# Optimization experiments

Measured on AMD Instinct MI355X. Metric: run time of the kernel, lower is better.

The kernel has to match this reference:

```python
import jax, jax.numpy as jnp
import numpy as np

B, S, E, H = 64, 512, 1024, 1024

def setup_inputs() -> dict:
    key = jax.random.key(0)
    k1, k2, k3, k4, k5 = jax.random.split(key, 5)
    emben_x = jax.random.normal(k1, (B, S, E), dtype=jnp.float32)
    sW = 1.0 / np.sqrt(E)
    sU = 1.0 / np.sqrt(H)
    W_w = jax.random.uniform(k2, (H, E), jnp.float32, -sW, sW)
    W_b = jax.random.uniform(k3, (H,), jnp.float32, -sW, sW)
    U_w = jax.random.uniform(k4, (H, H), jnp.float32, -sU, sU)
    U_b = jax.random.uniform(k5, (H,), jnp.float32, -sU, sU)
    return {"emben_x": emben_x, "W_w": W_w, "W_b": W_b, "U_w": U_w, "U_b": U_b}

def reference(emben_x, W_w, W_b, U_w, U_b):
    # Precompute input projection for all timesteps in one big GEMM: [B,S,H]
    wx = jnp.einsum('bse,he->bsh', emben_x, W_w) + W_b

    def step(t, wx_t):
        # h3 = tanh(W x_t + b_W + t); t_new = U h3 + b_U
        h3 = jnp.tanh(wx_t + t)
        t_new = h3 @ U_w.T + U_b
        return t_new, t_new

    t0 = jnp.zeros((emben_x.shape[0], U_w.shape[0]), dtype=emben_x.dtype)
    t_final, outs = jax.lax.scan(step, t0, jnp.swapaxes(wx, 0, 1))  # outs: [S,B,H]
    result1 = jnp.swapaxes(outs, 0, 1)  # [B,S,H]
    return result1, t_final
```

## Files before the change

### kernel.cpp

```cpp
#include <hip/hip_runtime.h>
#include <hip/hip_bf16.h>
#include <math.h>

#define RB 64
#define RS 512
#define RE 1024
#define RH 1024
#define BSH ((size_t)RB * RS * RH)

#define NBLK 256

typedef __attribute__((ext_vector_type(8))) __bf16 bf16x8;
typedef __attribute__((ext_vector_type(4))) float  f32x4;

__device__ __forceinline__ bf16x8 cvt8(f32x4 a, f32x4 b) {
    bf16x8 r;
    r[0] = (__bf16)a[0]; r[1] = (__bf16)a[1];
    r[2] = (__bf16)a[2]; r[3] = (__bf16)a[3];
    r[4] = (__bf16)b[0]; r[5] = (__bf16)b[1];
    r[6] = (__bf16)b[2]; r[7] = (__bf16)b[3];
    return r;
}

__device__ __forceinline__ bf16x8 ld_frag_agent(const unsigned long long* p) {
    union { unsigned long long u[2]; bf16x8 v; } r;
    r.u[0] = __hip_atomic_load(p,     __ATOMIC_RELAXED, __HIP_MEMORY_SCOPE_AGENT);
    r.u[1] = __hip_atomic_load(p + 1, __ATOMIC_RELAXED, __HIP_MEMORY_SCOPE_AGENT);
    return r.v;
}
__device__ __forceinline__ void st_bf16_agent(__bf16* p, float v) {
    union { __bf16 b; unsigned short s; } u;
    u.b = (__bf16)v;
    __hip_atomic_store(reinterpret_cast<unsigned short*>(p), u.s,
                       __ATOMIC_RELAXED, __HIP_MEMORY_SCOPE_AGENT);
}

__global__ void init_flags_k(unsigned* flags) {
    if (threadIdx.x < NBLK) flags[threadIdx.x] = 0u;
}

#define WBK  64
#define LDST 72

__global__ __launch_bounds__(256) void wx_gemm(
    const float* __restrict__ X,
    const float* __restrict__ Ww,
    const float* __restrict__ Wb,
    float* __restrict__ Out)
{
    __shared__ __align__(16) __bf16 As[128 * LDST];
    __shared__ __align__(16) __bf16 Bs[128 * LDST];

    const int tid  = threadIdx.x;
    const int lane = tid & 63;
    const int wave = tid >> 6;
    const int m0   = blockIdx.y * 128;
    const int n0   = blockIdx.x * 128;
    const int wm   = (wave >> 1) * 64;
    const int wn   = (wave & 1) * 64;

    const int sk   = (tid & 7) * 8;
    const int srow = tid >> 3;

    f32x4 acc[4][4];
#pragma unroll
    for (int i = 0; i < 4; ++i)
#pragma unroll
        for (int j = 0; j < 4; ++j) acc[i][j] = (f32x4){0.f, 0.f, 0.f, 0.f};

    for (int kc = 0; kc < RE; kc += WBK) {
#pragma unroll
        for (int rr = 0; rr < 128; rr += 32) {
            const float* xp = X + (size_t)(m0 + srow + rr) * RE + kc + sk;
            *reinterpret_cast<bf16x8*>(&As[(srow + rr) * LDST + sk]) =
                cvt8(*reinterpret_cast<const f32x4*>(xp),
                     *reinterpret_cast<const f32x4*>(xp + 4));
            const float* wp = Ww + (size_t)(n0 + srow + rr) * RE + kc + sk;
            *reinterpret_cast<bf16x8*>(&Bs[(srow + rr) * LDST + sk]) =
                cvt8(*reinterpret_cast<const f32x4*>(wp),
                     *reinterpret_cast<const f32x4*>(wp + 4));
        }
        __syncthreads();

#pragma unroll
        for (int ks = 0; ks < 2; ++ks) {
            bf16x8 af[4], bfr[4];
#pragma unroll
            for (int i = 0; i < 4; ++i) {
                af[i]  = *reinterpret_cast<const bf16x8*>(
                    &As[(wm + i * 16 + (lane & 15)) * LDST + ks * 32 + (lane >> 4) * 8]);
                bfr[i] = *reinterpret_cast<const bf16x8*>(
                    &Bs[(wn + i * 16 + (lane & 15)) * LDST + ks * 32 + (lane >> 4) * 8]);
            }
#pragma unroll
            for (int i = 0; i < 4; ++i)
#pragma unroll
                for (int j = 0; j < 4; ++j)
                    acc[i][j] = __builtin_amdgcn_mfma_f32_16x16x32_bf16(
                        af[i], bfr[j], acc[i][j], 0, 0, 0);
        }
        __syncthreads();
    }

    const int col = lane & 15, rbase = (lane >> 4) * 4;
#pragma unroll
    for (int j = 0; j < 4; ++j) {
        const int n = n0 + wn + j * 16 + col;
        const float bias = Wb[n];
#pragma unroll
        for (int i = 0; i < 4; ++i) {
#pragma unroll
            for (int r = 0; r < 4; ++r) {
                const int m = m0 + wm + i * 16 + rbase + r;
                Out[(size_t)m * RH + n] = acc[i][j][r] + bias;
            }
        }
    }
}

__global__ __launch_bounds__(256) void rnn_scan(
    const float* __restrict__ Uw,
    const float* __restrict__ Ub,
    float* Out,
    __bf16* hbuf,
    unsigned* flags)
{
    __shared__ float red[4 * 256];
    __shared__ float ubs[16];

    const int tid  = threadIdx.x;
    const int lane = tid & 63;
    const int wave = tid >> 6;
    const int bid  = blockIdx.x;
    const int cg   = bid >> 2;
    const int rg   = bid & 3;
    const int col0 = cg * 16;
    const int row0 = rg * 16;
    const int slot = rg * 64 + cg;

    bf16x8 ufr[8];
    {
        const float* up = Uw + (size_t)(col0 + (lane & 15)) * RH
                        + 256 * wave + ((lane >> 4) * 8);
#pragma unroll
        for (int j = 0; j < 8; ++j)
            ufr[j] = cvt8(*reinterpret_cast<const f32x4*>(up + j * 32),
                          *reinterpret_cast<const f32x4*>(up + j * 32 + 4));
    }
    if (tid < 16) ubs[tid] = Ub[col0 + tid];

    const int erow = row0 + (tid >> 4);
    const int ecol = col0 + (tid & 15);

    st_bf16_agent(hbuf + erow * RH + ecol,
                  tanhf(Out[(size_t)erow * RS * RH + ecol]));
    float wn_cur = Out[(size_t)erow * RS * RH + (size_t)1 * RH + ecol];
    __syncthreads();
    if (tid == 0)
        __hip_atomic_store(&flags[slot], 1u,
                           __ATOMIC_RELAXED, __HIP_MEMORY_SCOPE_AGENT);

    const int arow  = row0 + (lane & 15);
    const int kbase = 256 * wave + (lane >> 4) * 8;
    const unsigned* myflags = flags + rg * 64;

    for (int t = 0; t < RS; ++t) {
        const __bf16* cur = hbuf + (size_t)(t & 1) * (RB * RH);
        __bf16*       nxt = hbuf + (size_t)((t + 1) & 1) * (RB * RH);
        const unsigned long long* cp =
            reinterpret_cast<const unsigned long long*>(cur)
            + ((size_t)arow * RH + kbase) / 4;

        const unsigned tgt = (unsigned)(t + 1);
        while (true) {
            const unsigned f = __hip_atomic_load(&myflags[lane],
                                                 __ATOMIC_RELAXED,
                                                 __HIP_MEMORY_SCOPE_AGENT);
            if (__all(f >= tgt)) break;
            __builtin_amdgcn_s_sleep(1);
        }
        __builtin_amdgcn_sched_barrier(0);
        asm volatile("" ::: "memory");

        bf16x8 x0 = ld_frag_agent(cp + 0 * 8);
        bf16x8 x1 = ld_frag_agent(cp + 1 * 8);
        bf16x8 x2 = ld_frag_agent(cp + 2 * 8);
        bf16x8 x3 = ld_frag_agent(cp + 3 * 8);
        bf16x8 x4 = ld_frag_agent(cp + 4 * 8);
        bf16x8 x5 = ld_frag_agent(cp + 5 * 8);
        bf16x8 x6 = ld_frag_agent(cp + 6 * 8);
        bf16x8 x7 = ld_frag_agent(cp + 7 * 8);

        f32x4 ac0 = (f32x4){0.f, 0.f, 0.f, 0.f};
        f32x4 ac1 = ac0, ac2 = ac0, ac3 = ac0;
        ac0 = __builtin_amdgcn_mfma_f32_16x16x32_bf16(x0, ufr[0], ac0, 0, 0, 0);
        ac1 = __builtin_amdgcn_mfma_f32_16x16x32_bf16(x1, ufr[1], ac1, 0, 0, 0);
        ac2 = __builtin_amdgcn_mfma_f32_16x16x32_bf16(x2, ufr[2], ac2, 0, 0, 0);
        ac3 = __builtin_amdgcn_mfma_f32_16x16x32_bf16(x3, ufr[3], ac3, 0, 0, 0);
        ac0 = __builtin_amdgcn_mfma_f32_16x16x32_bf16(x4, ufr[4], ac0, 0, 0, 0);
        ac1 = __builtin_amdgcn_mfma_f32_16x16x32_bf16(x5, ufr[5], ac1, 0, 0, 0);
        ac2 = __builtin_amdgcn_mfma_f32_16x16x32_bf16(x6, ufr[6], ac2, 0, 0, 0);
        ac3 = __builtin_amdgcn_mfma_f32_16x16x32_bf16(x7, ufr[7], ac3, 0, 0, 0);
        const f32x4 acc = (ac0 + ac1) + (ac2 + ac3);

#pragma unroll
        for (int r = 0; r < 4; ++r)
            red[wave * 256 + ((lane >> 4) * 4 + r) * 16 + (lane & 15)] = acc[r];
        __syncthreads();

        const float v = red[tid] + red[256 + tid] + red[512 + tid] + red[768 + tid]
                      + ubs[tid & 15];
        const size_t oidx = (size_t)erow * RS * RH + (size_t)t * RH + ecol;
        if (t == RS - 1) {
            Out[oidx] = v;
            Out[BSH + (size_t)erow * RH + ecol] = v;
        } else {
            st_bf16_agent(nxt + erow * RH + ecol, tanhf(wn_cur + v));
            Out[oidx] = v;
            if (t < RS - 2)
                wn_cur = Out[(size_t)erow * RS * RH + (size_t)(t + 2) * RH + ecol];
            __syncthreads();
            if (tid == 0)
                __hip_atomic_store(&flags[slot], (unsigned)(t + 2),
                                   __ATOMIC_RELAXED, __HIP_MEMORY_SCOPE_AGENT);
        }
    }
}

extern "C" void kernel_launch(void* const* d_in, const int* in_sizes, int n_in,
                              void* d_out, int out_size, void* d_ws, size_t ws_size,
                              hipStream_t stream)
{
    const float* X  = (const float*)d_in[0];
    const float* Ww = (const float*)d_in[1];
    const float* Wb = (const float*)d_in[2];
    const float* Uw = (const float*)d_in[3];
    const float* Ub = (const float*)d_in[4];
    float* Out = (float*)d_out;

    __bf16* hbuf = (__bf16*)d_ws;
    unsigned* flags = (unsigned*)((char*)d_ws + (size_t)2 * RB * RH * sizeof(__bf16));

    hipLaunchKernelGGL(init_flags_k, dim3(1), dim3(256), 0, stream, flags);
    hipLaunchKernelGGL(wx_gemm, dim3(RH / 128, (RB * RS) / 128), dim3(256), 0, stream,
                       X, Ww, Wb, Out);
    hipLaunchKernelGGL(rnn_scan, dim3(NBLK), dim3(256), 0, stream,
                       Uw, Ub, Out, hbuf, flags);
}
```

Measured before the change: 2.242 ms.

## Shrink scan blocks to two waves and move output stores after flag release

The recurrent scan kernel now runs 128 threads per block. Each wave covers 512 of the K dimension with 16 MFMA fragments, so the cross-wave reduction sums two partials instead of four. Each thread handles two output rows. The reduction buffer is double-buffered by timestep parity, the next-step wx values are loaded before the spin-wait, and the global output stores happen after the flag is published. All of this shortens the per-step critical path between blocks. The cost is more registers per wave, twice as many serial MFMAs per wave, and fewer waves available to hide latency.

```diff
diff --git a/kernel.cpp b/kernel.cpp
--- a/kernel.cpp
+++ b/kernel.cpp
@@ -118,15 +118,14 @@
     }
 }
 
-__global__ __launch_bounds__(256) void rnn_scan(
+__global__ __launch_bounds__(128) void rnn_scan(
     const float* __restrict__ Uw,
     const float* __restrict__ Ub,
     float* Out,
     __bf16* hbuf,
     unsigned* flags)
 {
-    __shared__ float red[4 * 256];
-    __shared__ float ubs[16];
+    __shared__ float red[2][2][256];
 
     const int tid  = threadIdx.x;
     const int lane = tid & 63;
@@ -138,30 +137,34 @@
     const int row0 = rg * 16;
     const int slot = rg * 64 + cg;
 
-    bf16x8 ufr[8];
+    bf16x8 ufr[16];
     {
         const float* up = Uw + (size_t)(col0 + (lane & 15)) * RH
-                        + 256 * wave + ((lane >> 4) * 8);
-#pragma unroll
-        for (int j = 0; j < 8; ++j)
+                        + 512 * wave + ((lane >> 4) * 8);
+#pragma unroll
+        for (int j = 0; j < 16; ++j)
             ufr[j] = cvt8(*reinterpret_cast<const f32x4*>(up + j * 32),
                           *reinterpret_cast<const f32x4*>(up + j * 32 + 4));
     }
-    if (tid < 16) ubs[tid] = Ub[col0 + tid];
-
-    const int erow = row0 + (tid >> 4);
-    const int ecol = col0 + (tid & 15);
-
-    st_bf16_agent(hbuf + erow * RH + ecol,
-                  tanhf(Out[(size_t)erow * RS * RH + ecol]));
-    float wn_cur = Out[(size_t)erow * RS * RH + (size_t)1 * RH + ecol];
+
+    const int e0row = row0 + (tid >> 4);
+    const int e1row = e0row + 8;
+    const int ecol  = col0 + (tid & 15);
+    const float ub  = Ub[ecol];
+
+    {
+        const float w0 = Out[(size_t)e0row * RS * RH + ecol];
+        const float w1 = Out[(size_t)e1row * RS * RH + ecol];
+        st_bf16_agent(hbuf + e0row * RH + ecol, tanhf(w0));
+        st_bf16_agent(hbuf + e1row * RH + ecol, tanhf(w1));
+    }
     __syncthreads();
     if (tid == 0)
         __hip_atomic_store(&flags[slot], 1u,
                            __ATOMIC_RELAXED, __HIP_MEMORY_SCOPE_AGENT);
 
     const int arow  = row0 + (lane & 15);
-    const int kbase = 256 * wave + (lane >> 4) * 8;
+    const int kbase = 512 * wave + (lane >> 4) * 8;
     const unsigned* myflags = flags + rg * 64;
 
     for (int t = 0; t < RS; ++t) {
@@ -170,6 +173,12 @@
         const unsigned long long* cp =
             reinterpret_cast<const unsigned long long*>(cur)
             + ((size_t)arow * RH + kbase) / 4;
+
+        float wn0 = 0.f, wn1 = 0.f;
+        if (t < RS - 1) {
+            wn0 = Out[(size_t)e0row * RS * RH + (size_t)(t + 1) * RH + ecol];
+            wn1 = Out[(size_t)e1row * RS * RH + (size_t)(t + 1) * RH + ecol];
+        }
 
         const unsigned tgt = (unsigned)(t + 1);
         while (true) {
@@ -182,47 +191,50 @@
         __builtin_amdgcn_sched_barrier(0);
         asm volatile("" ::: "memory");
 
-        bf16x8 x0 = ld_frag_agent(cp + 0 * 8);
-        bf16x8 x1 = ld_frag_agent(cp + 1 * 8);
-        bf16x8 x2 = ld_frag_agent(cp + 2 * 8);
-        bf16x8 x3 = ld_frag_agent(cp + 3 * 8);
-        bf16x8 x4 = ld_frag_agent(cp + 4 * 8);
-        bf16x8 x5 = ld_frag_agent(cp + 5 * 8);
-        bf16x8 x6 = ld_frag_agent(cp + 6 * 8);
-        bf16x8 x7 = ld_frag_agent(cp + 7 * 8);
+        bf16x8 x[16];
+#pragma unroll
+        for (int f = 0; f < 16; ++f)
+            x[f] = ld_frag_agent(cp + f * 8);
 
         f32x4 ac0 = (f32x4){0.f, 0.f, 0.f, 0.f};
         f32x4 ac1 = ac0, ac2 = ac0, ac3 = ac0;
-        ac0 = __builtin_amdgcn_mfma_f32_16x16x32_bf16(x0, ufr[0], ac0, 0, 0, 0);
-        ac1 = __builtin_amdgcn_mfma_f32_16x16x32_bf16(x1, ufr[1], ac1, 0, 0, 0);
-        ac2 = __builtin_amdgcn_mfma_f32_16x16x32_bf16(x2, ufr[2], ac2, 0, 0, 0);
-        ac3 = __builtin_amdgcn_mfma_f32_16x16x32_bf16(x3, ufr[3], ac3, 0, 0, 0);
-        ac0 = __builtin_amdgcn_mfma_f32_16x16x32_bf16(x4, ufr[4], ac0, 0, 0, 0);
-        ac1 = __builtin_amdgcn_mfma_f32_16x16x32_bf16(x5, ufr[5], ac1, 0, 0, 0);
-        ac2 = __builtin_amdgcn_mfma_f32_16x16x32_bf16(x6, ufr[6], ac2, 0, 0, 0);
-        ac3 = __builtin_amdgcn_mfma_f32_16x16x32_bf16(x7, ufr[7], ac3, 0, 0, 0);
+#pragma unroll
+        for (int f = 0; f < 16; f += 4) {
+            ac0 = __builtin_amdgcn_mfma_f32_16x16x32_bf16(x[f + 0], ufr[f + 0], ac0, 0, 0, 0);
+            ac1 = __builtin_amdgcn_mfma_f32_16x16x32_bf16(x[f + 1], ufr[f + 1], ac1, 0, 0, 0);
+            ac2 = __builtin_amdgcn_mfma_f32_16x16x32_bf16(x[f + 2], ufr[f + 2], ac2, 0, 0, 0);
+            ac3 = __builtin_amdgcn_mfma_f32_16x16x32_bf16(x[f + 3], ufr[f + 3], ac3, 0, 0, 0);
+        }
         const f32x4 acc = (ac0 + ac1) + (ac2 + ac3);
 
-#pragma unroll
-        for (int r = 0; r < 4; ++r)
-            red[wave * 256 + ((lane >> 4) * 4 + r) * 16 + (lane & 15)] = acc[r];
+        {
+            float* rb = red[t & 1][wave];
+#pragma unroll
+            for (int r = 0; r < 4; ++r)
+                rb[((lane >> 4) * 4 + r) * 16 + (lane & 15)] = acc[r];
+        }
         __syncthreads();
-
-        const float v = red[tid] + red[256 + tid] + red[512 + tid] + red[768 + tid]
-                      + ubs[tid & 15];
-        const size_t oidx = (size_t)erow * RS * RH + (size_t)t * RH + ecol;
+        const float* r0 = red[t & 1][0];
+        const float* r1 = red[t & 1][1];
+        const float v0 = r0[tid]       + r1[tid]       + ub;
+        const float v1 = r0[tid + 128] + r1[tid + 128] + ub;
+
+        const size_t o0 = (size_t)e0row * RS * RH + (size_t)t * RH + ecol;
+        const size_t o1 = (size_t)e1row * RS * RH + (size_t)t * RH + ecol;
         if (t == RS - 1) {
-            Out[oidx] = v;
-            Out[BSH + (size_t)erow * RH + ecol] = v;
+            Out[o0] = v0;
+            Out[o1] = v1;
+            Out[BSH + (size_t)e0row * RH + ecol] = v0;
+            Out[BSH + (size_t)e1row * RH + ecol] = v1;
         } else {
-            st_bf16_agent(nxt + erow * RH + ecol, tanhf(wn_cur + v));
-            Out[oidx] = v;
-            if (t < RS - 2)
-                wn_cur = Out[(size_t)erow * RS * RH + (size_t)(t + 2) * RH + ecol];
+            st_bf16_agent(nxt + e0row * RH + ecol, tanhf(wn0 + v0));
+            st_bf16_agent(nxt + e1row * RH + ecol, tanhf(wn1 + v1));
             __syncthreads();
             if (tid == 0)
                 __hip_atomic_store(&flags[slot], (unsigned)(t + 2),
                                    __ATOMIC_RELAXED, __HIP_MEMORY_SCOPE_AGENT);
+            Out[o0] = v0;
+            Out[o1] = v1;
         }
     }
 }
@@ -244,6 +256,6 @@
     hipLaunchKernelGGL(init_flags_k, dim3(1), dim3(256), 0, stream, flags);
     hipLaunchKernelGGL(wx_gemm, dim3(RH / 128, (RB * RS) / 128), dim3(256), 0, stream,
                        X, Ww, Wb, Out);
-    hipLaunchKernelGGL(rnn_scan, dim3(NBLK), dim3(256), 0, stream,
+    hipLaunchKernelGGL(rnn_scan, dim3(NBLK), dim3(128), 0, stream,
                        Uw, Ub, Out, hbuf, flags);
 }
```

New measurement: 2.245 ms. No clear change (+0.1%).

## Replace per-block flag barrier with step-tagged hidden-state words in scan

Applied to the files above, without the earlier changes.

Each hidden-state element is now stored as a 32-bit word that packs the bf16 value with the timestep tag in its upper half. Consumers spin directly on the data words until every tag matches the current step, which removes the per-block flag store and the extra __syncthreads around it. The reduction buffer is double-buffered so the next step can begin without waiting on a barrier. In exchange, each step reads twice the bytes, has to unpack the values in registers, and the tag region needs a wider init kernel.

```diff
diff --git a/kernel.cpp b/kernel.cpp
--- a/kernel.cpp
+++ b/kernel.cpp
@@ -22,21 +22,10 @@
     return r;
 }
 
-__device__ __forceinline__ bf16x8 ld_frag_agent(const unsigned long long* p) {
-    union { unsigned long long u[2]; bf16x8 v; } r;
-    r.u[0] = __hip_atomic_load(p,     __ATOMIC_RELAXED, __HIP_MEMORY_SCOPE_AGENT);
-    r.u[1] = __hip_atomic_load(p + 1, __ATOMIC_RELAXED, __HIP_MEMORY_SCOPE_AGENT);
-    return r.v;
-}
-__device__ __forceinline__ void st_bf16_agent(__bf16* p, float v) {
-    union { __bf16 b; unsigned short s; } u;
-    u.b = (__bf16)v;
-    __hip_atomic_store(reinterpret_cast<unsigned short*>(p), u.s,
-                       __ATOMIC_RELAXED, __HIP_MEMORY_SCOPE_AGENT);
-}
-
-__global__ void init_flags_k(unsigned* flags) {
-    if (threadIdx.x < NBLK) flags[threadIdx.x] = 0u;
+__global__ __launch_bounds__(256) void init_tags_k(unsigned* tbuf) {
+    const int i = blockIdx.x * 256 + threadIdx.x;
+    tbuf[i]         = 0xFFFF0000u;
+    tbuf[i + 65536] = 0xFFFF0000u;
 }
 
 #define WBK  64
@@ -118,14 +107,13 @@
     }
 }
 
-__global__ __launch_bounds__(256) void rnn_scan(
+__global__ __launch_bounds__(256, 1) void rnn_scan_tag(
     const float* __restrict__ Uw,
     const float* __restrict__ Ub,
     float* Out,
-    __bf16* hbuf,
-    unsigned* flags)
+    unsigned* tbuf)
 {
-    __shared__ float red[4 * 256];
+    __shared__ float red[2][4 * 256];
     __shared__ float ubs[16];
 
     const int tid  = threadIdx.x;
@@ -136,7 +124,6 @@
     const int rg   = bid & 3;
     const int col0 = cg * 16;
     const int row0 = rg * 16;
-    const int slot = rg * 64 + cg;
 
     bf16x8 ufr[8];
     {
@@ -152,77 +139,89 @@
     const int erow = row0 + (tid >> 4);
     const int ecol = col0 + (tid & 15);
 
-    st_bf16_agent(hbuf + erow * RH + ecol,
-                  tanhf(Out[(size_t)erow * RS * RH + ecol]));
+    {
+        const float w = Out[(size_t)erow * RS * RH + ecol];
+        union { __bf16 b; unsigned short s; } u; u.b = (__bf16)tanhf(w);
+        __hip_atomic_store(&tbuf[(size_t)erow * RH + ecol], (unsigned)u.s,
+                           __ATOMIC_RELAXED, __HIP_MEMORY_SCOPE_AGENT);
+    }
     float wn_cur = Out[(size_t)erow * RS * RH + (size_t)1 * RH + ecol];
-    __syncthreads();
-    if (tid == 0)
-        __hip_atomic_store(&flags[slot], 1u,
-                           __ATOMIC_RELAXED, __HIP_MEMORY_SCOPE_AGENT);
 
     const int arow  = row0 + (lane & 15);
     const int kbase = 256 * wave + (lane >> 4) * 8;
-    const unsigned* myflags = flags + rg * 64;
 
     for (int t = 0; t < RS; ++t) {
-        const __bf16* cur = hbuf + (size_t)(t & 1) * (RB * RH);
-        __bf16*       nxt = hbuf + (size_t)((t + 1) & 1) * (RB * RH);
+        const unsigned* cur = tbuf + (size_t)(t & 1) * (RB * RH);
+        unsigned*       nxt = tbuf + (size_t)((t + 1) & 1) * (RB * RH);
         const unsigned long long* cp =
             reinterpret_cast<const unsigned long long*>(cur)
-            + ((size_t)arow * RH + kbase) / 4;
-
-        const unsigned tgt = (unsigned)(t + 1);
+            + ((size_t)arow * RH + kbase) / 2;
+
+        const unsigned long long half = ((unsigned long long)(unsigned)t) << 16;
+        const unsigned long long rep  = half | (half << 32);
+        const unsigned long long hm   = 0xFFFF0000FFFF0000ull;
+
+        unsigned long long q[32];
         while (true) {
-            const unsigned f = __hip_atomic_load(&myflags[lane],
-                                                 __ATOMIC_RELAXED,
-                                                 __HIP_MEMORY_SCOPE_AGENT);
-            if (__all(f >= tgt)) break;
+#pragma unroll
+            for (int j = 0; j < 32; ++j)
+                q[j] = __hip_atomic_load(cp + (size_t)(j >> 2) * 16 + (j & 3),
+                                         __ATOMIC_RELAXED,
+                                         __HIP_MEMORY_SCOPE_AGENT);
+            unsigned long long bad = 0;
+#pragma unroll
+            for (int j = 0; j < 32; ++j) { q[j] ^= rep; bad |= q[j]; }
+            if (__all((bad & hm) == 0ull)) break;
             __builtin_amdgcn_s_sleep(1);
         }
-        __builtin_amdgcn_sched_barrier(0);
-        asm volatile("" ::: "memory");
-
-        bf16x8 x0 = ld_frag_agent(cp + 0 * 8);
-        bf16x8 x1 = ld_frag_agent(cp + 1 * 8);
-        bf16x8 x2 = ld_frag_agent(cp + 2 * 8);
-        bf16x8 x3 = ld_frag_agent(cp + 3 * 8);
-        bf16x8 x4 = ld_frag_agent(cp + 4 * 8);
-        bf16x8 x5 = ld_frag_agent(cp + 5 * 8);
-        bf16x8 x6 = ld_frag_agent(cp + 6 * 8);
-        bf16x8 x7 = ld_frag_agent(cp + 7 * 8);
+
+        bf16x8 xf[8];
+#pragma unroll
+        for (int f = 0; f < 8; ++f) {
+            union { unsigned u[4]; bf16x8 v; } w;
+#pragma unroll
+            for (int i = 0; i < 4; ++i) {
+                const unsigned long long y = q[f * 4 + i];
+                const unsigned lo = (unsigned)y;
+                const unsigned hi = (unsigned)(y >> 32);
+                w.u[i] = lo | (hi << 16);
+            }
+            xf[f] = w.v;
+        }
 
         f32x4 ac0 = (f32x4){0.f, 0.f, 0.f, 0.f};
         f32x4 ac1 = ac0, ac2 = ac0, ac3 = ac0;
-        ac0 = __builtin_amdgcn_mfma_f32_16x16x32_bf16(x0, ufr[0], ac0, 0, 0, 0);
-        ac1 = __builtin_amdgcn_mfma_f32_16x16x32_bf16(x1, ufr[1], ac1, 0, 0, 0);
-        ac2 = __builtin_amdgcn_mfma_f32_16x16x32_bf16(x2, ufr[2], ac2, 0, 0, 0);
-        ac3 = __builtin_amdgcn_mfma_f32_16x16x32_bf16(x3, ufr[3], ac3, 0, 0, 0);
-        ac0 = __builtin_amdgcn_mfma_f32_16x16x32_bf16(x4, ufr[4], ac0, 0, 0, 0);
-        ac1 = __builtin_amdgcn_mfma_f32_16x16x32_bf16(x5, ufr[5], ac1, 0, 0, 0);
-        ac2 = __builtin_amdgcn_mfma_f32_16x16x32_bf16(x6, ufr[6], ac2, 0, 0, 0);
-        ac3 = __builtin_amdgcn_mfma_f32_16x16x32_bf16(x7, ufr[7], ac3, 0, 0, 0);
+        ac0 = __builtin_amdgcn_mfma_f32_16x16x32_bf16(xf[0], ufr[0], ac0, 0, 0, 0);
+        ac1 = __builtin_amdgcn_mfma_f32_16x16x32_bf16(xf[1], ufr[1], ac1, 0, 0, 0);
+        ac2 = __builtin_amdgcn_mfma_f32_16x16x32_bf16(xf[2], ufr[2], ac2, 0, 0, 0);
+        ac3 = __builtin_amdgcn_mfma_f32_16x16x32_bf16(xf[3], ufr[3], ac3, 0, 0, 0);
+        ac0 = __builtin_amdgcn_mfma_f32_16x16x32_bf16(xf[4], ufr[4], ac0, 0, 0, 0);
+        ac1 = __builtin_amdgcn_mfma_f32_16x16x32_bf16(xf[5], ufr[5], ac1, 0, 0, 0);
+        ac2 = __builtin_amdgcn_mfma_f32_16x16x32_bf16(xf[6], ufr[6], ac2, 0, 0, 0);
+        ac3 = __builtin_amdgcn_mfma_f32_16x16x32_bf16(xf[7], ufr[7], ac3, 0, 0, 0);
         const f32x4 acc = (ac0 + ac1) + (ac2 + ac3);
 
+        float* rb = red[t & 1];
 #pragma unroll
         for (int r = 0; r < 4; ++r)
-            red[wave * 256 + ((lane >> 4) * 4 + r) * 16 + (lane & 15)] = acc[r];
+            rb[wave * 256 + ((lane >> 4) * 4 + r) * 16 + (lane & 15)] = acc[r];
         __syncthreads();
 
-        const float v = red[tid] + red[256 + tid] + red[512 + tid] + red[768 + tid]
+        const float v = rb[tid] + rb[256 + tid] + rb[512 + tid] + rb[768 + tid]
                       + ubs[tid & 15];
         const size_t oidx = (size_t)erow * RS * RH + (size_t)t * RH + ecol;
         if (t == RS - 1) {
             Out[oidx] = v;
             Out[BSH + (size_t)erow * RH + ecol] = v;
         } else {
-            st_bf16_agent(nxt + erow * RH + ecol, tanhf(wn_cur + v));
+            const float h = tanhf(wn_cur + v);
+            union { __bf16 b; unsigned short s; } u; u.b = (__bf16)h;
+            const unsigned tv = ((unsigned)(t + 1) << 16) | (unsigned)u.s;
+            __hip_atomic_store(&nxt[(size_t)erow * RH + ecol], tv,
+                               __ATOMIC_RELAXED, __HIP_MEMORY_SCOPE_AGENT);
             Out[oidx] = v;
             if (t < RS - 2)
                 wn_cur = Out[(size_t)erow * RS * RH + (size_t)(t + 2) * RH + ecol];
-            __syncthreads();
-            if (tid == 0)
-                __hip_atomic_store(&flags[slot], (unsigned)(t + 2),
-                                   __ATOMIC_RELAXED, __HIP_MEMORY_SCOPE_AGENT);
         }
     }
 }
@@ -238,12 +237,11 @@
     const float* Ub = (const float*)d_in[4];
     float* Out = (float*)d_out;
 
-    __bf16* hbuf = (__bf16*)d_ws;
-    unsigned* flags = (unsigned*)((char*)d_ws + (size_t)2 * RB * RH * sizeof(__bf16));
-
-    hipLaunchKernelGGL(init_flags_k, dim3(1), dim3(256), 0, stream, flags);
+    unsigned* tbuf = (unsigned*)d_ws;
+
+    hipLaunchKernelGGL(init_tags_k, dim3(256), dim3(256), 0, stream, tbuf);
     hipLaunchKernelGGL(wx_gemm, dim3(RH / 128, (RB * RS) / 128), dim3(256), 0, stream,
                        X, Ww, Wb, Out);
-    hipLaunchKernelGGL(rnn_scan, dim3(NBLK), dim3(256), 0, stream,
-                       Uw, Ub, Out, hbuf, flags);
-}
+    hipLaunchKernelGGL(rnn_scan_tag, dim3(NBLK), dim3(256), 0, stream,
+                       Uw, Ub, Out, tbuf);
+}
```

New measurement: 3.585 ms. 59.9% more time.

## Process all four batch row groups per scan block with 64 blocks

Applied to the files above, without the earlier changes.

The recurrent scan now runs on 64 blocks instead of 256. Each block owns a 16-column slice and handles all 64 batch rows as four 16-row chains, loading the next chain's hidden-state fragments while the current one computes. Fewer blocks means each block polls 64 flags instead of fewer participants per group, and the grid-wide flag handshake involves fewer producers. The cost is four times more serial MFMA and reduction work per block per step, plus the output stores and wx prefetch are moved after the flag publish.

```diff
diff --git a/kernel.cpp b/kernel.cpp
--- a/kernel.cpp
+++ b/kernel.cpp
@@ -8,7 +8,7 @@
 #define RH 1024
 #define BSH ((size_t)RB * RS * RH)
 
-#define NBLK 256
+#define NBLK_SCAN 64
 
 typedef __attribute__((ext_vector_type(8))) __bf16 bf16x8;
 typedef __attribute__((ext_vector_type(4))) float  f32x4;
@@ -36,7 +36,7 @@
 }
 
 __global__ void init_flags_k(unsigned* flags) {
-    if (threadIdx.x < NBLK) flags[threadIdx.x] = 0u;
+    if (threadIdx.x < 256) flags[threadIdx.x] = 0u;
 }
 
 #define WBK  64
@@ -118,25 +118,48 @@
     }
 }
 
-__global__ __launch_bounds__(256) void rnn_scan(
+
+#define CHAIN_COMPUTE(RG, X)                                                    \
+    {                                                                           \
+        f32x4 ac0 = (f32x4){0.f, 0.f, 0.f, 0.f};                                \
+        f32x4 ac1 = ac0, ac2 = ac0, ac3 = ac0;                                  \
+        ac0 = __builtin_amdgcn_mfma_f32_16x16x32_bf16(X[0], ufr[0], ac0, 0,0,0);\
+        ac1 = __builtin_amdgcn_mfma_f32_16x16x32_bf16(X[1], ufr[1], ac1, 0,0,0);\
+        ac2 = __builtin_amdgcn_mfma_f32_16x16x32_bf16(X[2], ufr[2], ac2, 0,0,0);\
+        ac3 = __builtin_amdgcn_mfma_f32_16x16x32_bf16(X[3], ufr[3], ac3, 0,0,0);\
+        ac0 = __builtin_amdgcn_mfma_f32_16x16x32_bf16(X[4], ufr[4], ac0, 0,0,0);\
+        ac1 = __builtin_amdgcn_mfma_f32_16x16x32_bf16(X[5], ufr[5], ac1, 0,0,0);\
+        ac2 = __builtin_amdgcn_mfma_f32_16x16x32_bf16(X[6], ufr[6], ac2, 0,0,0);\
+        ac3 = __builtin_amdgcn_mfma_f32_16x16x32_bf16(X[7], ufr[7], ac3, 0,0,0);\
+        const f32x4 accv = (ac0 + ac1) + (ac2 + ac3);                           \
+        float* rb = red[(RG) & 1];                                              \
+        _Pragma("unroll")                                                       \
+        for (int r = 0; r < 4; ++r)                                             \
+            rb[wave * 256 + ((lane >> 4) * 4 + r) * 16 + (lane & 15)] = accv[r];\
+        __syncthreads();                                                        \
+        const float v = rb[tid] + rb[256 + tid] + rb[512 + tid] + rb[768 + tid] \
+                      + ubs[tid & 15];                                          \
+        vout[RG] = v;                                                           \
+        if (s < RS - 1)                                                         \
+            st_bf16_agent(nxt + ((RG) * 16 + er) * RH + ecol,                   \
+                          tanhf(wn[RG] + v));                                   \
+    }
+
+__global__ __launch_bounds__(256, 1) void rnn_scan4(
     const float* __restrict__ Uw,
     const float* __restrict__ Ub,
     float* Out,
     __bf16* hbuf,
     unsigned* flags)
 {
-    __shared__ float red[4 * 256];
+    __shared__ float red[2][4 * 256];
     __shared__ float ubs[16];
 
     const int tid  = threadIdx.x;
     const int lane = tid & 63;
     const int wave = tid >> 6;
-    const int bid  = blockIdx.x;
-    const int cg   = bid >> 2;
-    const int rg   = bid & 3;
+    const int cg   = blockIdx.x;
     const int col0 = cg * 16;
-    const int row0 = rg * 16;
-    const int slot = rg * 64 + cg;
 
     bf16x8 ufr[8];
     {
@@ -149,31 +172,32 @@
     }
     if (tid < 16) ubs[tid] = Ub[col0 + tid];
 
-    const int erow = row0 + (tid >> 4);
+    const int er   = tid >> 4;
     const int ecol = col0 + (tid & 15);
 
-    st_bf16_agent(hbuf + erow * RH + ecol,
-                  tanhf(Out[(size_t)erow * RS * RH + ecol]));
-    float wn_cur = Out[(size_t)erow * RS * RH + (size_t)1 * RH + ecol];
+    float wn[4];
+#pragma unroll
+    for (int rg = 0; rg < 4; ++rg) {
+        const int erow = rg * 16 + er;
+        const float w = Out[(size_t)erow * RS * RH + ecol];
+        st_bf16_agent(hbuf + erow * RH + ecol, tanhf(w));
+        wn[rg] = Out[(size_t)erow * RS * RH + (size_t)1 * RH + ecol];
+    }
     __syncthreads();
     if (tid == 0)
-        __hip_atomic_store(&flags[slot], 1u,
+        __hip_atomic_store(&flags[cg], 1u,
                            __ATOMIC_RELAXED, __HIP_MEMORY_SCOPE_AGENT);
 
-    const int arow  = row0 + (lane & 15);
-    const int kbase = 256 * wave + (lane >> 4) * 8;
-    const unsigned* myflags = flags + rg * 64;
-
-    for (int t = 0; t < RS; ++t) {
-        const __bf16* cur = hbuf + (size_t)(t & 1) * (RB * RH);
-        __bf16*       nxt = hbuf + (size_t)((t + 1) & 1) * (RB * RH);
-        const unsigned long long* cp =
-            reinterpret_cast<const unsigned long long*>(cur)
-            + ((size_t)arow * RH + kbase) / 4;
-
-        const unsigned tgt = (unsigned)(t + 1);
+    const int arow_in = lane & 15;
+    const int kbase   = 256 * wave + (lane >> 4) * 8;
+
+    for (int s = 0; s < RS; ++s) {
+        const __bf16* cur = hbuf + (size_t)(s & 1) * (RB * RH);
+        __bf16*       nxt = hbuf + (size_t)((s + 1) & 1) * (RB * RH);
+
+        const unsigned tgt = (unsigned)(s + 1);
         while (true) {
-            const unsigned f = __hip_atomic_load(&myflags[lane],
+            const unsigned f = __hip_atomic_load(&flags[lane],
                                                  __ATOMIC_RELAXED,
                                                  __HIP_MEMORY_SCOPE_AGENT);
             if (__all(f >= tgt)) break;
@@ -182,47 +206,46 @@
         __builtin_amdgcn_sched_barrier(0);
         asm volatile("" ::: "memory");
 
-        bf16x8 x0 = ld_frag_agent(cp + 0 * 8);
-        bf16x8 x1 = ld_frag_agent(cp + 1 * 8);
-        bf16x8 x2 = ld_frag_agent(cp + 2 * 8);
-        bf16x8 x3 = ld_frag_agent(cp + 3 * 8);
-        bf16x8 x4 = ld_frag_agent(cp + 4 * 8);
-        bf16x8 x5 = ld_frag_agent(cp + 5 * 8);
-        bf16x8 x6 = ld_frag_agent(cp + 6 * 8);
-        bf16x8 x7 = ld_frag_agent(cp + 7 * 8);
-
-        f32x4 ac0 = (f32x4){0.f, 0.f, 0.f, 0.f};
-        f32x4 ac1 = ac0, ac2 = ac0, ac3 = ac0;
-        ac0 = __builtin_amdgcn_mfma_f32_16x16x32_bf16(x0, ufr[0], ac0, 0, 0, 0);
-        ac1 = __builtin_amdgcn_mfma_f32_16x16x32_bf16(x1, ufr[1], ac1, 0, 0, 0);
-        ac2 = __builtin_amdgcn_mfma_f32_16x16x32_bf16(x2, ufr[2], ac2, 0, 0, 0);
-        ac3 = __builtin_amdgcn_mfma_f32_16x16x32_bf16(x3, ufr[3], ac3, 0, 0, 0);
-        ac0 = __builtin_amdgcn_mfma_f32_16x16x32_bf16(x4, ufr[4], ac0, 0, 0, 0);
-        ac1 = __builtin_amdgcn_mfma_f32_16x16x32_bf16(x5, ufr[5], ac1, 0, 0, 0);
-        ac2 = __builtin_amdgcn_mfma_f32_16x16x32_bf16(x6, ufr[6], ac2, 0, 0, 0);
-        ac3 = __builtin_amdgcn_mfma_f32_16x16x32_bf16(x7, ufr[7], ac3, 0, 0, 0);
-        const f32x4 acc = (ac0 + ac1) + (ac2 + ac3);
-
-#pragma unroll
-        for (int r = 0; r < 4; ++r)
-            red[wave * 256 + ((lane >> 4) * 4 + r) * 16 + (lane & 15)] = acc[r];
-        __syncthreads();
-
-        const float v = red[tid] + red[256 + tid] + red[512 + tid] + red[768 + tid]
-                      + ubs[tid & 15];
-        const size_t oidx = (size_t)erow * RS * RH + (size_t)t * RH + ecol;
-        if (t == RS - 1) {
-            Out[oidx] = v;
-            Out[BSH + (size_t)erow * RH + ecol] = v;
-        } else {
-            st_bf16_agent(nxt + erow * RH + ecol, tanhf(wn_cur + v));
-            Out[oidx] = v;
-            if (t < RS - 2)
-                wn_cur = Out[(size_t)erow * RS * RH + (size_t)(t + 2) * RH + ecol];
+        const unsigned long long* cp0 = reinterpret_cast<const unsigned long long*>(cur)
+            + ((size_t)(0 * 16 + arow_in) * RH + kbase) / 4;
+        const unsigned long long* cp1 = reinterpret_cast<const unsigned long long*>(cur)
+            + ((size_t)(1 * 16 + arow_in) * RH + kbase) / 4;
+        const unsigned long long* cp2 = reinterpret_cast<const unsigned long long*>(cur)
+            + ((size_t)(2 * 16 + arow_in) * RH + kbase) / 4;
+        const unsigned long long* cp3 = reinterpret_cast<const unsigned long long*>(cur)
+            + ((size_t)(3 * 16 + arow_in) * RH + kbase) / 4;
+
+        float vout[4];
+        bf16x8 xA[8], xB[8];
+
+#pragma unroll
+        for (int f = 0; f < 8; ++f) xA[f] = ld_frag_agent(cp0 + f * 8);
+#pragma unroll
+        for (int f = 0; f < 8; ++f) xB[f] = ld_frag_agent(cp1 + f * 8);
+        CHAIN_COMPUTE(0, xA)
+#pragma unroll
+        for (int f = 0; f < 8; ++f) xA[f] = ld_frag_agent(cp2 + f * 8);
+        CHAIN_COMPUTE(1, xB)
+#pragma unroll
+        for (int f = 0; f < 8; ++f) xB[f] = ld_frag_agent(cp3 + f * 8);
+        CHAIN_COMPUTE(2, xA)
+        CHAIN_COMPUTE(3, xB)
+
+        if (s < RS - 1) {
             __syncthreads();
             if (tid == 0)
-                __hip_atomic_store(&flags[slot], (unsigned)(t + 2),
+                __hip_atomic_store(&flags[cg], (unsigned)(s + 2),
                                    __ATOMIC_RELAXED, __HIP_MEMORY_SCOPE_AGENT);
+        }
+
+#pragma unroll
+        for (int rg = 0; rg < 4; ++rg) {
+            const int erow = rg * 16 + er;
+            Out[(size_t)erow * RS * RH + (size_t)s * RH + ecol] = vout[rg];
+            if (s == RS - 1)
+                Out[BSH + (size_t)erow * RH + ecol] = vout[rg];
+            else if (s < RS - 2)
+                wn[rg] = Out[(size_t)erow * RS * RH + (size_t)(s + 2) * RH + ecol];
         }
     }
 }
@@ -244,6 +267,6 @@
     hipLaunchKernelGGL(init_flags_k, dim3(1), dim3(256), 0, stream, flags);
     hipLaunchKernelGGL(wx_gemm, dim3(RH / 128, (RB * RS) / 128), dim3(256), 0, stream,
                        X, Ww, Wb, Out);
-    hipLaunchKernelGGL(rnn_scan, dim3(NBLK), dim3(256), 0, stream,
+    hipLaunchKernelGGL(rnn_scan4, dim3(NBLK_SCAN), dim3(256), 0, stream,
                        Uw, Ub, Out, hbuf, flags);
 }
```

After: 5.229 ms. 133% more time.
